# Optimization experiments

Measured on AMD Instinct MI355X. Metric: run time of the kernel, lower is better.

The kernel has to match this reference:

```python
import jax, jax.numpy as jnp
import numpy as np

HIDDEN = 16
ROUNDS = 5


def _mlp2(x, W1, b1, W2, b2):
    # features-first MLP: x [in, E] -> [out, E]
    h = jax.nn.relu(W1 @ x + b1[:, None])
    return W2 @ h + b2[:, None]


def setup_inputs() -> dict:
    key = jax.random.key(0)
    ks = jax.random.split(key, 20)
    n_nodes, n_edges, n_bi, h = 100_000, 1_000_000, 500_000, HIDDEN

    def lin(k, o, i):
        return (jax.random.normal(k, (o, i), jnp.float32) / float(np.sqrt(i)))

    inp = {
        "nodes": jax.random.normal(ks[0], (n_nodes,), jnp.float32),
        "edges": jax.random.normal(ks[1], (n_edges,), jnp.float32),
        "receivers": jax.random.randint(ks[2], (n_edges,), 0, n_nodes),
        "senders": jax.random.randint(ks[3], (n_edges,), 0, n_nodes),
        "bi_edges_indx": jax.random.randint(ks[4], (2, n_bi), 0, n_edges),
        # NodeEncoder: 1 -> h -> h
        "node_enc_W1": lin(ks[5], h, 1), "node_enc_b1": jnp.zeros(h, jnp.float32),
        "node_enc_W2": lin(ks[6], h, h), "node_enc_b2": jnp.zeros(h, jnp.float32),
        # EdgeEncoder: 1 -> h -> h
        "edge_enc_W1": lin(ks[7], h, 1), "edge_enc_b1": jnp.zeros(h, jnp.float32),
        "edge_enc_W2": lin(ks[8], h, h), "edge_enc_b2": jnp.zeros(h, jnp.float32),
        # MessagePass (per-round weights): edge update 3h->h->h, node update 2h->h->h
        "mp_edge_W1": jax.random.normal(ks[9], (ROUNDS, h, 3 * h), jnp.float32) / float(np.sqrt(3 * h)),
        "mp_edge_b1": jnp.zeros((ROUNDS, h), jnp.float32),
        "mp_edge_W2": jax.random.normal(ks[10], (ROUNDS, h, h), jnp.float32) / float(np.sqrt(h)),
        "mp_edge_b2": jnp.zeros((ROUNDS, h), jnp.float32),
        "mp_node_W1": jax.random.normal(ks[11], (ROUNDS, h, 2 * h), jnp.float32) / float(np.sqrt(2 * h)),
        "mp_node_b1": jnp.zeros((ROUNDS, h), jnp.float32),
        "mp_node_W2": jax.random.normal(ks[12], (ROUNDS, h, h), jnp.float32) / float(np.sqrt(h)),
        "mp_node_b2": jnp.zeros((ROUNDS, h), jnp.float32),
        # EdgeDecoder: h -> h -> 1
        "edge_dec_W1": lin(ks[13], h, h), "edge_dec_b1": jnp.zeros(h, jnp.float32),
        "edge_dec_W2": lin(ks[14], 1, h), "edge_dec_b2": jnp.zeros(1, jnp.float32),
    }
    return inp


def reference(nodes, edges, receivers, senders, bi_edges_indx,
              node_enc_W1, node_enc_b1, node_enc_W2, node_enc_b2,
              edge_enc_W1, edge_enc_b1, edge_enc_W2, edge_enc_b2,
              mp_edge_W1, mp_edge_b1, mp_edge_W2, mp_edge_b2,
              mp_node_W1, mp_node_b1, mp_node_W2, mp_node_b2,
              edge_dec_W1, edge_dec_b1, edge_dec_W2, edge_dec_b2):
    n_nodes = nodes.shape[0]
    # encode (features-first layout, eqx Linear semantics W @ x)
    nf = _mlp2(nodes[None, :], node_enc_W1, node_enc_b1, node_enc_W2, node_enc_b2)  # [h, n_nodes]
    ef = _mlp2(edges[None, :], edge_enc_W1, edge_enc_b1, edge_enc_W2, edge_enc_b2)  # [h, n_edges]

    ones = jnp.ones((ef.shape[1],), ef.dtype)
    deg = jnp.maximum(jax.ops.segment_sum(ones, receivers, num_segments=n_nodes), 1.0)

    for r in range(ROUNDS):
        # edge update: gather sender/receiver node feats, MLP on concat [3h, E]
        msg_in = jnp.concatenate([nf[:, senders], nf[:, receivers], ef], axis=0)
        ef = _mlp2(msg_in, mp_edge_W1[r], mp_edge_b1[r], mp_edge_W2[r], mp_edge_b2[r])
        # node update: scatter-average incoming edges then MLP on concat [2h, N]
        agg = jax.ops.segment_sum(ef.T, receivers, num_segments=n_nodes).T / deg[None, :]
        nf = _mlp2(jnp.concatenate([nf, agg], axis=0), mp_node_W1[r], mp_node_b1[r], mp_node_W2[r], mp_node_b2[r])

    # bidirectional edge averaging: avg (i->j, j->i) pairs
    i, j = bi_edges_indx[0], bi_edges_indx[1]
    avg = 0.5 * (ef[:, i] + ef[:, j])
    ef = ef.at[:, i].set(avg).at[:, j].set(avg)

    # decode to scalar edge values, squeeze
    vals = _mlp2(ef, edge_dec_W1, edge_dec_b1, edge_dec_W2, edge_dec_b2)[0]  # [n_edges]

    # graph_tril: keep lower-triangular entries (row=receiver >= col=sender), zero the rest
    vals = jnp.where(receivers >= senders, vals, jnp.zeros((), vals.dtype))
    # COO representation of the lower-triangular sparse matrix (data, rows, cols)
    return vals, receivers, senders
```

## Files before the change

### kernel.cpp

```cpp
#include <hip/hip_runtime.h>
#include <hip/hip_bf16.h>

#define H 16
#define NW 20
#define SCAN_TILE 2048

typedef __attribute__((ext_vector_type(8))) short short8;
typedef __attribute__((ext_vector_type(4))) float f32x4;

__device__ __forceinline__ float bf2f(unsigned short u) {
    union { unsigned int u; float f; } c; c.u = ((unsigned int)u) << 16; return c.f;
}

__device__ __forceinline__ unsigned short f2bf(float f) {
    union { float f; unsigned int u; } c; c.f = f;
    unsigned int u = c.u;
    unsigned int r = (u + 0x7fffu + ((u >> 16) & 1u)) >> 16;
    return (unsigned short)r;
}

__device__ __forceinline__ unsigned int packbf2(float a, float b) {
    return (unsigned int)f2bf(a) | ((unsigned int)f2bf(b) << 16);
}

__device__ __forceinline__ void unpack8(uint4 u, float* f) {
    union { unsigned int u; float f; } c;
    c.u = u.x << 16; f[0] = c.f; c.u = u.x & 0xffff0000u; f[1] = c.f;
    c.u = u.y << 16; f[2] = c.f; c.u = u.y & 0xffff0000u; f[3] = c.f;
    c.u = u.z << 16; f[4] = c.f; c.u = u.z & 0xffff0000u; f[5] = c.f;
    c.u = u.w << 16; f[6] = c.f; c.u = u.w & 0xffff0000u; f[7] = c.f;
}

struct WPtrs { const unsigned short* src[NW]; int len[NW]; int off[NW]; };

__global__ void cvt_weights_kernel(WPtrs p, float* __restrict__ dst) {
    int a = blockIdx.x;
    const unsigned short* s = p.src[a];
    float* d = dst + p.off[a];
    int n = p.len[a];
    for (int t = threadIdx.x; t < n; t += blockDim.x) d[t] = bf2f(s[t]);
}

__global__ void mk_frags_kernel(const unsigned short* __restrict__ W1raw,
                                const unsigned short* __restrict__ W2raw,
                                unsigned short* __restrict__ w1a,
                                unsigned short* __restrict__ w2a)
{
    for (int idx = threadIdx.x; idx < 5 * 2 * 64 * 8; idx += blockDim.x) {
        int j = idx & 7, l = (idx >> 3) & 63, c = (idx >> 9) & 1, r = idx >> 10;
        int m = l & 15, quad = l >> 4;
        int k = c * 32 + quad * 8 + j;
        w1a[idx] = (k < 48) ? W1raw[(r * 16 + m) * 48 + k] : (unsigned short)0;
    }
    for (int idx = threadIdx.x; idx < 5 * 64 * 8; idx += blockDim.x) {
        int j = idx & 7, l = (idx >> 3) & 63, r = idx >> 9;
        int m = l & 15, quad = l >> 4;
        int k = quad * 8 + j;
        w2a[idx] = (k < 16) ? W2raw[(r * 16 + m) * 16 + k] : (unsigned short)0;
    }
}

__global__ __launch_bounds__(256) void encode_node_kernel(
    const unsigned short* __restrict__ xin, int n,
    const float* __restrict__ W1, const float* __restrict__ b1,
    const float* __restrict__ W2, const float* __restrict__ b2,
    unsigned short* __restrict__ out)
{
    int i = blockIdx.x * blockDim.x + threadIdx.x;
    if (i >= n) return;
    float v = bf2f(xin[i]);
    float h[H];
    #pragma unroll
    for (int o = 0; o < H; ++o) {
        float t = W1[o] * v + b1[o];
        h[o] = t > 0.f ? t : 0.f;
    }
    float acc[H];
    #pragma unroll
    for (int o = 0; o < H; ++o) acc[o] = b2[o];
    #pragma unroll
    for (int k = 0; k < H; ++k) {
        float hk = h[k];
        #pragma unroll
        for (int o = 0; o < H; ++o) acc[o] += W2[o * H + k] * hk;
    }
    uint4 o0, o1;
    o0.x = packbf2(acc[0], acc[1]);  o0.y = packbf2(acc[2], acc[3]);
    o0.z = packbf2(acc[4], acc[5]);  o0.w = packbf2(acc[6], acc[7]);
    o1.x = packbf2(acc[8], acc[9]);  o1.y = packbf2(acc[10], acc[11]);
    o1.z = packbf2(acc[12], acc[13]); o1.w = packbf2(acc[14], acc[15]);
    uint4* dst = (uint4*)(out + (size_t)i * H);
    dst[0] = o0; dst[1] = o1;
}

__global__ __launch_bounds__(256) void encode_edge_kernel(
    const unsigned short* __restrict__ edges, const int* __restrict__ elist, int n_edges,
    const float* __restrict__ W1, const float* __restrict__ b1,
    const float* __restrict__ W2, const float* __restrict__ b2,
    unsigned short* __restrict__ efb)
{
    int pos = blockIdx.x * blockDim.x + threadIdx.x;
    if (pos >= n_edges) return;
    float v = bf2f(edges[elist[pos]]);
    float h[H];
    #pragma unroll
    for (int o = 0; o < H; ++o) {
        float t = W1[o] * v + b1[o];
        h[o] = t > 0.f ? t : 0.f;
    }
    float acc[H];
    #pragma unroll
    for (int o = 0; o < H; ++o) acc[o] = b2[o];
    #pragma unroll
    for (int k = 0; k < H; ++k) {
        float hk = h[k];
        #pragma unroll
        for (int o = 0; o < H; ++o) acc[o] += W2[o * H + k] * hk;
    }
    uint4 o0, o1;
    o0.x = packbf2(acc[0], acc[1]);  o0.y = packbf2(acc[2], acc[3]);
    o0.z = packbf2(acc[4], acc[5]);  o0.w = packbf2(acc[6], acc[7]);
    o1.x = packbf2(acc[8], acc[9]);  o1.y = packbf2(acc[10], acc[11]);
    o1.z = packbf2(acc[12], acc[13]); o1.w = packbf2(acc[14], acc[15]);
    uint4* dst = (uint4*)(efb + (size_t)pos * H);
    dst[0] = o0; dst[1] = o1;
}

__global__ __launch_bounds__(256) void hist_kernel(
    const int* __restrict__ recv, int n_edges, int* __restrict__ cnt)
{
    int e = blockIdx.x * blockDim.x + threadIdx.x;
    if (e < n_edges) atomicAdd(&cnt[recv[e]], 1);
}

__global__ __launch_bounds__(256) void scan_part_kernel(
    const int* __restrict__ cnt, int n, int* __restrict__ blocksum)
{
    int base = blockIdx.x * SCAN_TILE + threadIdx.x * 8;
    int s = 0;
    #pragma unroll
    for (int k = 0; k < 8; ++k) { int i = base + k; if (i < n) s += cnt[i]; }
    __shared__ int red[256];
    red[threadIdx.x] = s;
    __syncthreads();
    for (int off = 128; off > 0; off >>= 1) {
        if (threadIdx.x < off) red[threadIdx.x] += red[threadIdx.x + off];
        __syncthreads();
    }
    if (threadIdx.x == 0) blocksum[blockIdx.x] = red[0];
}

__global__ __launch_bounds__(1024) void scan_blocksums_kernel(
    int* __restrict__ blocksum, int nb, int n, int* __restrict__ row_start)
{
    __shared__ int sums[1024];
    int t = threadIdx.x;
    int v = (t < nb) ? blocksum[t] : 0;
    sums[t] = v;
    __syncthreads();
    for (int off = 1; off < 1024; off <<= 1) {
        int u = (t >= off) ? sums[t - off] : 0;
        __syncthreads();
        sums[t] += u;
        __syncthreads();
    }
    if (t < nb) blocksum[t] = sums[t] - v;
    if (t == 1023) row_start[n] = sums[1023];
}

__global__ __launch_bounds__(256) void scan_final_kernel(
    const int* __restrict__ cnt, int n, const int* __restrict__ blocksum,
    int* __restrict__ row_start, int* __restrict__ cursor)
{
    int t = threadIdx.x;
    int base = blockIdx.x * SCAN_TILE + t * 8;
    int loc[8]; int s = 0;
    #pragma unroll
    for (int k = 0; k < 8; ++k) { int i = base + k; loc[k] = (i < n) ? cnt[i] : 0; s += loc[k]; }
    __shared__ int sums[256];
    sums[t] = s;
    __syncthreads();
    for (int off = 1; off < 256; off <<= 1) {
        int u = (t >= off) ? sums[t - off] : 0;
        __syncthreads();
        sums[t] += u;
        __syncthreads();
    }
    int run = blocksum[blockIdx.x] + sums[t] - s;
    #pragma unroll
    for (int k = 0; k < 8; ++k) {
        int i = base + k;
        if (i < n) { row_start[i] = run; cursor[i] = run; run += loc[k]; }
    }
}

__global__ __launch_bounds__(256) void fill_kernel(
    const int* __restrict__ recv, const int* __restrict__ send, int n_edges,
    int* __restrict__ cursor, int* __restrict__ elist, int* __restrict__ ipos,
    int* __restrict__ s_perm, int* __restrict__ r_perm)
{
    int e = blockIdx.x * blockDim.x + threadIdx.x;
    if (e >= n_edges) return;
    int r = recv[e];
    int pos = atomicAdd(&cursor[r], 1);
    elist[pos] = e;
    ipos[e] = pos;
    s_perm[pos] = send[e];
    r_perm[pos] = r;
}

__global__ __launch_bounds__(256) void edge_update_mfma(
    const unsigned short* __restrict__ nfb, unsigned short* __restrict__ efb,
    const int* __restrict__ s_perm, const int* __restrict__ r_perm, int n_edges,
    const unsigned short* __restrict__ w1a, const unsigned short* __restrict__ w2a,
    const float* __restrict__ b1, const float* __restrict__ b2)
{
    __shared__ uint4 Xs[8 * 256];
    __shared__ uint4 Hs[4 * 4 * 16];

    const int t = threadIdx.x;
    const int lane = t & 63;
    const int wave = t >> 6;
    const int quad = lane >> 4;
    const int nn = lane & 15;
    const int base = blockIdx.x * 256;

    const short8 wa0 = *(const short8*)(w1a + (size_t)lane * 8);
    const short8 wa1 = *(const short8*)(w1a + 512 + (size_t)lane * 8);
    const short8 wa2 = *(const short8*)(w2a + (size_t)lane * 8);
    const float4 bv1 = *(const float4*)(b1 + quad * 4);
    const float4 bv2 = *(const float4*)(b2 + quad * 4);

    int pos = base + t;
    int cp = pos < n_edges ? pos : n_edges - 1;
    int s = s_perm[cp], r = r_perm[cp];
    const uint4* pns = (const uint4*)(nfb + (size_t)s * H);
    const uint4* pnr = (const uint4*)(nfb + (size_t)r * H);
    const uint4* pef = (const uint4*)(efb + (size_t)cp * H);
    uint4 a0 = pns[0], a1 = pns[1];
    uint4 r0 = pnr[0], r1 = pnr[1];
    uint4 c0 = pef[0], c1 = pef[1];
    uint4 z; z.x = 0; z.y = 0; z.z = 0; z.w = 0;
    Xs[0 * 256 + t] = a0; Xs[1 * 256 + t] = a1;
    Xs[2 * 256 + t] = r0; Xs[3 * 256 + t] = r1;
    Xs[4 * 256 + t] = c0; Xs[5 * 256 + t] = c1;
    Xs[6 * 256 + t] = z;  Xs[7 * 256 + t] = z;
    if (lane < 32) Hs[wave * 64 + 32 + lane] = z;
    __syncthreads();

    #pragma unroll
    for (int it = 0; it < 4; ++it) {
        int nb = it * 64 + wave * 16 + nn;
        const short8 xb0 = *(const short8*)&Xs[quad * 256 + nb];
        const short8 xb1 = *(const short8*)&Xs[(4 + quad) * 256 + nb];
        f32x4 d1 = {0.f, 0.f, 0.f, 0.f};
        d1 = __builtin_amdgcn_mfma_f32_16x16x32_bf16(wa0, xb0, d1, 0, 0, 0);
        d1 = __builtin_amdgcn_mfma_f32_16x16x32_bf16(wa1, xb1, d1, 0, 0, 0);
        float h0 = d1[0] + bv1.x; h0 = h0 > 0.f ? h0 : 0.f;
        float h1 = d1[1] + bv1.y; h1 = h1 > 0.f ? h1 : 0.f;
        float h2 = d1[2] + bv1.z; h2 = h2 > 0.f ? h2 : 0.f;
        float h3 = d1[3] + bv1.w; h3 = h3 > 0.f ? h3 : 0.f;
        uint2 hu;
        hu.x = packbf2(h0, h1);
        hu.y = packbf2(h2, h3);
        ((uint2*)Hs)[(wave * 64 + (quad >> 1) * 16 + nn) * 2 + (quad & 1)] = hu;
        __syncthreads();
        const short8 hb = *(const short8*)&Hs[wave * 64 + quad * 16 + nn];
        f32x4 d2 = {0.f, 0.f, 0.f, 0.f};
        d2 = __builtin_amdgcn_mfma_f32_16x16x32_bf16(wa2, hb, d2, 0, 0, 0);
        int edge = base + nb;
        if (edge < n_edges) {
            uint2 ov;
            ov.x = packbf2(d2[0] + bv2.x, d2[1] + bv2.y);
            ov.y = packbf2(d2[2] + bv2.z, d2[3] + bv2.w);
            ((uint2*)efb)[(size_t)edge * 4 + quad] = ov;
        }
        __syncthreads();
    }
}

__global__ __launch_bounds__(256) void node_update_kernel(
    unsigned short* __restrict__ nfb, const unsigned short* __restrict__ ef,
    const int* __restrict__ row_start, int n_nodes,
    const float* __restrict__ W1, const float* __restrict__ b1,
    const float* __restrict__ W2, const float* __restrict__ b2)
{
    int i = blockIdx.x * blockDim.x + threadIdx.x;
    if (i >= n_nodes) return;
    int lo = row_start[i], hi = row_start[i + 1];
    float a[H];
    #pragma unroll
    for (int o = 0; o < H; ++o) a[o] = 0.f;
    for (int j = lo; j < hi; ++j) {
        const uint4* pe = (const uint4*)(ef + (size_t)j * H);
        uint4 u0 = pe[0], u1 = pe[1];
        float f[H];
        unpack8(u0, f);
        unpack8(u1, f + 8);
        #pragma unroll
        for (int o = 0; o < H; ++o) a[o] += f[o];
    }
    int d = hi - lo;
    float rd = 1.0f / (float)(d > 1 ? d : 1);

    const uint4* pn = (const uint4*)(nfb + (size_t)i * H);
    uint4 n0 = pn[0], n1 = pn[1];
    float xn[H];
    unpack8(n0, xn);
    unpack8(n1, xn + 8);

    float h[H];
    #pragma unroll
    for (int o = 0; o < H; ++o) h[o] = b1[o];
    #pragma unroll
    for (int k = 0; k < H; ++k) {
        float xk = xn[k];
        #pragma unroll
        for (int o = 0; o < H; ++o) h[o] += W1[o * 32 + k] * xk;
    }
    #pragma unroll
    for (int k = 0; k < H; ++k) {
        float xk = a[k] * rd;
        #pragma unroll
        for (int o = 0; o < H; ++o) h[o] += W1[o * 32 + 16 + k] * xk;
    }
    #pragma unroll
    for (int o = 0; o < H; ++o) h[o] = h[o] > 0.f ? h[o] : 0.f;
    float acc[H];
    #pragma unroll
    for (int o = 0; o < H; ++o) acc[o] = b2[o];
    #pragma unroll
    for (int k = 0; k < H; ++k) {
        float hk = h[k];
        #pragma unroll
        for (int o = 0; o < H; ++o) acc[o] += W2[o * H + k] * hk;
    }
    uint4 o0, o1;
    o0.x = packbf2(acc[0], acc[1]);  o0.y = packbf2(acc[2], acc[3]);
    o0.z = packbf2(acc[4], acc[5]);  o0.w = packbf2(acc[6], acc[7]);
    o1.x = packbf2(acc[8], acc[9]);  o1.y = packbf2(acc[10], acc[11]);
    o1.z = packbf2(acc[12], acc[13]); o1.w = packbf2(acc[14], acc[15]);
    uint4* dst = (uint4*)(nfb + (size_t)i * H);
    dst[0] = o0; dst[1] = o1;
}

__global__ __launch_bounds__(256) void bi_avg_kernel(
    unsigned short* __restrict__ ef, const int* __restrict__ ipos,
    const int* __restrict__ bi, int n_bi)
{
    int p = blockIdx.x * blockDim.x + threadIdx.x;
    if (p >= n_bi) return;
    int i = ipos[bi[p]], j = ipos[bi[n_bi + p]];
    uint4* pi = (uint4*)(ef + (size_t)i * H);
    uint4* pj = (uint4*)(ef + (size_t)j * H);
    uint4 a0 = pi[0], a1 = pi[1], b0 = pj[0], b1 = pj[1];
    float fa[H], fb[H];
    unpack8(a0, fa); unpack8(a1, fa + 8);
    unpack8(b0, fb); unpack8(b1, fb + 8);
    float m[H];
    #pragma unroll
    for (int o = 0; o < H; ++o) m[o] = 0.5f * (fa[o] + fb[o]);
    uint4 o0, o1;
    o0.x = packbf2(m[0], m[1]);  o0.y = packbf2(m[2], m[3]);
    o0.z = packbf2(m[4], m[5]);  o0.w = packbf2(m[6], m[7]);
    o1.x = packbf2(m[8], m[9]);  o1.y = packbf2(m[10], m[11]);
    o1.z = packbf2(m[12], m[13]); o1.w = packbf2(m[14], m[15]);
    pi[0] = o0; pi[1] = o1;
    pj[0] = o0; pj[1] = o1;
}

__global__ __launch_bounds__(256) void decode_kernel(
    const unsigned short* __restrict__ ef, const int* __restrict__ ipos,
    const int* __restrict__ recv, const int* __restrict__ send, int n_edges,
    const float* __restrict__ W1, const float* __restrict__ b1,
    const float* __restrict__ W2, const float* __restrict__ b2,
    float* __restrict__ out)
{
    int e = blockIdx.x * blockDim.x + threadIdx.x;
    if (e >= n_edges) return;
    int pos = ipos[e];
    const uint4* pe = (const uint4*)(ef + (size_t)pos * H);
    uint4 u0 = pe[0], u1 = pe[1];
    float x[H];
    unpack8(u0, x);
    unpack8(u1, x + 8);
    float h[H];
    #pragma unroll
    for (int o = 0; o < H; ++o) h[o] = b1[o];
    #pragma unroll
    for (int k = 0; k < H; ++k) {
        float xk = x[k];
        #pragma unroll
        for (int o = 0; o < H; ++o) h[o] += W1[o * H + k] * xk;
    }
    float val = b2[0];
    #pragma unroll
    for (int k = 0; k < H; ++k) {
        float hk = h[k] > 0.f ? h[k] : 0.f;
        val += W2[k] * hk;
    }
    int r = recv[e], s = send[e];
    val = (r >= s) ? val : 0.0f;
    out[e] = val;
    out[(size_t)n_edges + e] = bf2f(f2bf((float)r));
    out[2 * (size_t)n_edges + e] = bf2f(f2bf((float)s));
}

extern "C" void kernel_launch(void* const* d_in, const int* in_sizes, int n_in,
                              void* d_out, int out_size, void* d_ws, size_t ws_size,
                              hipStream_t stream) {
    const unsigned short* nodes = (const unsigned short*)d_in[0];
    const unsigned short* edges = (const unsigned short*)d_in[1];
    const int* receivers = (const int*)d_in[2];
    const int* senders   = (const int*)d_in[3];
    const int* bi        = (const int*)d_in[4];
    const int n_nodes = in_sizes[0];
    const int n_edges = in_sizes[1];
    const int n_bi    = in_sizes[4] / 2;

    static const int wl[NW] = {16,16,256,16, 16,16,256,16,
                               3840,80,1280,80, 2560,80,1280,80,
                               256,16,16,1};
    WPtrs wp;
    {
        int off = 0;
        for (int a = 0; a < NW; ++a) {
            wp.src[a] = (const unsigned short*)d_in[5 + a];
            wp.len[a] = wl[a];
            wp.off[a] = off;
            off += wl[a];
        }
    }
    float* wf = (float*)d_ws;
    const float* Wf[NW];
    for (int a = 0; a < NW; ++a) Wf[a] = wf + wp.off[a];

    unsigned short* w1a = (unsigned short*)(wf + 10240);
    unsigned short* w2a = w1a + 5 * 2 * 64 * 8;
    unsigned short* nfb = w2a + 5 * 64 * 8;
    unsigned short* efb = nfb + (size_t)n_nodes * H;
    int* cnt       = (int*)(efb + (size_t)n_edges * H);
    int* row_start = cnt + n_nodes;
    int* cursor    = row_start + n_nodes + 1;
    int* elist     = cursor + n_nodes;
    int* ipos      = elist + n_edges;
    int* s_perm    = ipos + n_edges;
    int* r_perm    = s_perm + n_edges;
    int* blocksum  = r_perm + n_edges;

    const int bn = 256;
    const int nb_scan = (n_nodes + SCAN_TILE - 1) / SCAN_TILE;
    const int nb_edge = (n_edges + bn - 1) / bn;

    cvt_weights_kernel<<<NW, 256, 0, stream>>>(wp, wf);
    mk_frags_kernel<<<1, 256, 0, stream>>>(
        (const unsigned short*)d_in[13], (const unsigned short*)d_in[15], w1a, w2a);
    encode_node_kernel<<<(n_nodes + bn - 1) / bn, bn, 0, stream>>>(
        nodes, n_nodes, Wf[0], Wf[1], Wf[2], Wf[3], nfb);

    hipMemsetAsync(cnt, 0, (size_t)n_nodes * 4, stream);
    hist_kernel<<<nb_edge, bn, 0, stream>>>(receivers, n_edges, cnt);
    scan_part_kernel<<<nb_scan, 256, 0, stream>>>(cnt, n_nodes, blocksum);
    scan_blocksums_kernel<<<1, 1024, 0, stream>>>(blocksum, nb_scan, n_nodes, row_start);
    scan_final_kernel<<<nb_scan, 256, 0, stream>>>(cnt, n_nodes, blocksum, row_start, cursor);
    fill_kernel<<<nb_edge, bn, 0, stream>>>(
        receivers, senders, n_edges, cursor, elist, ipos, s_perm, r_perm);

    encode_edge_kernel<<<nb_edge, bn, 0, stream>>>(
        edges, elist, n_edges, Wf[4], Wf[5], Wf[6], Wf[7], efb);

    for (int r = 0; r < 5; ++r) {
        edge_update_mfma<<<nb_edge, bn, 0, stream>>>(
            nfb, efb, s_perm, r_perm, n_edges,
            w1a + r * 1024, w2a + r * 512,
            Wf[9] + r * H, Wf[11] + r * H);
        node_update_kernel<<<(n_nodes + bn - 1) / bn, bn, 0, stream>>>(
            nfb, efb, row_start, n_nodes,
            Wf[12] + r * 2 * H * H, Wf[13] + r * H,
            Wf[14] + r * H * H,     Wf[15] + r * H);
    }

    bi_avg_kernel<<<(n_bi + bn - 1) / bn, bn, 0, stream>>>(efb, ipos, bi, n_bi);
    decode_kernel<<<nb_edge, bn, 0, stream>>>(
        efb, ipos, receivers, senders, n_edges,
        Wf[16], Wf[17], Wf[18], Wf[19], (float*)d_out);
}
```

Before: 514.7 us.

## Fuse segment aggregation into edge update kernel via shared-memory partial sums

The edge-update kernel now writes its bf16 outputs into shared memory and sums edges per receiver within each 256-edge block, writing fp32 partials to an agg buffer. Receivers whose edge range lies entirely inside the block get a plain store; ranges that cross a block boundary use atomics. The node update then reads the 16 precomputed sums per node instead of walking its CSR edge list over efb. The sender is now fetched indirectly through elist and senders instead of a materialised s_perm, and r_perm is built by a separate expand kernel. In exchange, each round adds a memset of agg and an extra indirection in the edge kernel, and boundary atomics make the summation order vary between runs.

```diff
diff --git a/kernel.cpp b/kernel.cpp
--- a/kernel.cpp
+++ b/kernel.cpp
@@ -93,6 +93,94 @@
     dst[0] = o0; dst[1] = o1;
 }
 
+__global__ __launch_bounds__(256) void hist_kernel(
+    const int* __restrict__ recv, int n_edges, int* __restrict__ cnt)
+{
+    int e = blockIdx.x * blockDim.x + threadIdx.x;
+    if (e < n_edges) atomicAdd(&cnt[recv[e]], 1);
+}
+
+__global__ __launch_bounds__(256) void scan_part_kernel(
+    const int* __restrict__ cnt, int n, int* __restrict__ blocksum)
+{
+    int base = blockIdx.x * SCAN_TILE + threadIdx.x * 8;
+    int s = 0;
+    #pragma unroll
+    for (int k = 0; k < 8; ++k) { int i = base + k; if (i < n) s += cnt[i]; }
+    __shared__ int red[256];
+    red[threadIdx.x] = s;
+    __syncthreads();
+    for (int off = 128; off > 0; off >>= 1) {
+        if (threadIdx.x < off) red[threadIdx.x] += red[threadIdx.x + off];
+        __syncthreads();
+    }
+    if (threadIdx.x == 0) blocksum[blockIdx.x] = red[0];
+}
+
+__global__ __launch_bounds__(1024) void scan_blocksums_kernel(
+    int* __restrict__ blocksum, int nb, int n, int* __restrict__ row_start)
+{
+    __shared__ int sums[1024];
+    int t = threadIdx.x;
+    int v = (t < nb) ? blocksum[t] : 0;
+    sums[t] = v;
+    __syncthreads();
+    for (int off = 1; off < 1024; off <<= 1) {
+        int u = (t >= off) ? sums[t - off] : 0;
+        __syncthreads();
+        sums[t] += u;
+        __syncthreads();
+    }
+    if (t < nb) blocksum[t] = sums[t] - v;
+    if (t == 1023) row_start[n] = sums[1023];
+}
+
+__global__ __launch_bounds__(256) void scan_final_kernel(
+    const int* __restrict__ cnt, int n, const int* __restrict__ blocksum,
+    int* __restrict__ row_start, int* __restrict__ cursor)
+{
+    int t = threadIdx.x;
+    int base = blockIdx.x * SCAN_TILE + t * 8;
+    int loc[8]; int s = 0;
+    #pragma unroll
+    for (int k = 0; k < 8; ++k) { int i = base + k; loc[k] = (i < n) ? cnt[i] : 0; s += loc[k]; }
+    __shared__ int sums[256];
+    sums[t] = s;
+    __syncthreads();
+    for (int off = 1; off < 256; off <<= 1) {
+        int u = (t >= off) ? sums[t - off] : 0;
+        __syncthreads();
+        sums[t] += u;
+        __syncthreads();
+    }
+    int run = blocksum[blockIdx.x] + sums[t] - s;
+    #pragma unroll
+    for (int k = 0; k < 8; ++k) {
+        int i = base + k;
+        if (i < n) { row_start[i] = run; cursor[i] = run; run += loc[k]; }
+    }
+}
+
+__global__ __launch_bounds__(256) void expand_r_kernel(
+    const int* __restrict__ row_start, int n_nodes, int* __restrict__ r_perm)
+{
+    int i = blockIdx.x * blockDim.x + threadIdx.x;
+    if (i >= n_nodes) return;
+    int lo = row_start[i], hi = row_start[i + 1];
+    for (int p = lo; p < hi; ++p) r_perm[p] = i;
+}
+
+__global__ __launch_bounds__(256) void fill_kernel(
+    const int* __restrict__ recv, int n_edges,
+    int* __restrict__ cursor, int* __restrict__ ipos, int* __restrict__ elist)
+{
+    int e = blockIdx.x * blockDim.x + threadIdx.x;
+    if (e >= n_edges) return;
+    int pos = atomicAdd(&cursor[recv[e]], 1);
+    ipos[e] = pos;
+    elist[pos] = e;
+}
+
 __global__ __launch_bounds__(256) void encode_edge_kernel(
     const unsigned short* __restrict__ edges, const int* __restrict__ elist, int n_edges,
     const float* __restrict__ W1, const float* __restrict__ b1,
@@ -126,92 +214,11 @@
     dst[0] = o0; dst[1] = o1;
 }
 
-__global__ __launch_bounds__(256) void hist_kernel(
-    const int* __restrict__ recv, int n_edges, int* __restrict__ cnt)
-{
-    int e = blockIdx.x * blockDim.x + threadIdx.x;
-    if (e < n_edges) atomicAdd(&cnt[recv[e]], 1);
-}
-
-__global__ __launch_bounds__(256) void scan_part_kernel(
-    const int* __restrict__ cnt, int n, int* __restrict__ blocksum)
-{
-    int base = blockIdx.x * SCAN_TILE + threadIdx.x * 8;
-    int s = 0;
-    #pragma unroll
-    for (int k = 0; k < 8; ++k) { int i = base + k; if (i < n) s += cnt[i]; }
-    __shared__ int red[256];
-    red[threadIdx.x] = s;
-    __syncthreads();
-    for (int off = 128; off > 0; off >>= 1) {
-        if (threadIdx.x < off) red[threadIdx.x] += red[threadIdx.x + off];
-        __syncthreads();
-    }
-    if (threadIdx.x == 0) blocksum[blockIdx.x] = red[0];
-}
-
-__global__ __launch_bounds__(1024) void scan_blocksums_kernel(
-    int* __restrict__ blocksum, int nb, int n, int* __restrict__ row_start)
-{
-    __shared__ int sums[1024];
-    int t = threadIdx.x;
-    int v = (t < nb) ? blocksum[t] : 0;
-    sums[t] = v;
-    __syncthreads();
-    for (int off = 1; off < 1024; off <<= 1) {
-        int u = (t >= off) ? sums[t - off] : 0;
-        __syncthreads();
-        sums[t] += u;
-        __syncthreads();
-    }
-    if (t < nb) blocksum[t] = sums[t] - v;
-    if (t == 1023) row_start[n] = sums[1023];
-}
-
-__global__ __launch_bounds__(256) void scan_final_kernel(
-    const int* __restrict__ cnt, int n, const int* __restrict__ blocksum,
-    int* __restrict__ row_start, int* __restrict__ cursor)
-{
-    int t = threadIdx.x;
-    int base = blockIdx.x * SCAN_TILE + t * 8;
-    int loc[8]; int s = 0;
-    #pragma unroll
-    for (int k = 0; k < 8; ++k) { int i = base + k; loc[k] = (i < n) ? cnt[i] : 0; s += loc[k]; }
-    __shared__ int sums[256];
-    sums[t] = s;
-    __syncthreads();
-    for (int off = 1; off < 256; off <<= 1) {
-        int u = (t >= off) ? sums[t - off] : 0;
-        __syncthreads();
-        sums[t] += u;
-        __syncthreads();
-    }
-    int run = blocksum[blockIdx.x] + sums[t] - s;
-    #pragma unroll
-    for (int k = 0; k < 8; ++k) {
-        int i = base + k;
-        if (i < n) { row_start[i] = run; cursor[i] = run; run += loc[k]; }
-    }
-}
-
-__global__ __launch_bounds__(256) void fill_kernel(
-    const int* __restrict__ recv, const int* __restrict__ send, int n_edges,
-    int* __restrict__ cursor, int* __restrict__ elist, int* __restrict__ ipos,
-    int* __restrict__ s_perm, int* __restrict__ r_perm)
-{
-    int e = blockIdx.x * blockDim.x + threadIdx.x;
-    if (e >= n_edges) return;
-    int r = recv[e];
-    int pos = atomicAdd(&cursor[r], 1);
-    elist[pos] = e;
-    ipos[e] = pos;
-    s_perm[pos] = send[e];
-    r_perm[pos] = r;
-}
-
 __global__ __launch_bounds__(256) void edge_update_mfma(
     const unsigned short* __restrict__ nfb, unsigned short* __restrict__ efb,
-    const int* __restrict__ s_perm, const int* __restrict__ r_perm, int n_edges,
+    const int* __restrict__ elist, const int* __restrict__ senders,
+    const int* __restrict__ r_perm, const int* __restrict__ row_start,
+    float* __restrict__ agg, int n_edges,
     const unsigned short* __restrict__ w1a, const unsigned short* __restrict__ w2a,
     const float* __restrict__ b1, const float* __restrict__ b2)
 {
@@ -233,7 +240,9 @@
 
     int pos = base + t;
     int cp = pos < n_edges ? pos : n_edges - 1;
-    int s = s_perm[cp], r = r_perm[cp];
+    int e = elist[cp];
+    int s = senders[e];
+    int r = r_perm[cp];
     const uint4* pns = (const uint4*)(nfb + (size_t)s * H);
     const uint4* pnr = (const uint4*)(nfb + (size_t)r * H);
     const uint4* pef = (const uint4*)(efb + (size_t)cp * H);
@@ -268,40 +277,63 @@
         const short8 hb = *(const short8*)&Hs[wave * 64 + quad * 16 + nn];
         f32x4 d2 = {0.f, 0.f, 0.f, 0.f};
         d2 = __builtin_amdgcn_mfma_f32_16x16x32_bf16(wa2, hb, d2, 0, 0, 0);
+        uint2 ov;
+        ov.x = packbf2(d2[0] + bv2.x, d2[1] + bv2.y);
+        ov.y = packbf2(d2[2] + bv2.z, d2[3] + bv2.w);
         int edge = base + nb;
-        if (edge < n_edges) {
-            uint2 ov;
-            ov.x = packbf2(d2[0] + bv2.x, d2[1] + bv2.y);
-            ov.y = packbf2(d2[2] + bv2.z, d2[3] + bv2.w);
+        if (edge < n_edges)
             ((uint2*)efb)[(size_t)edge * 4 + quad] = ov;
+        ((uint2*)Xs)[((quad >> 1) * 256 + nb) * 2 + (quad & 1)] = ov;
+        __syncthreads();
+    }
+
+    int last = (base + 255 < n_edges) ? base + 255 : n_edges - 1;
+    int r_lo = r_perm[base];
+    int r_hi = r_perm[last];
+    int npairs = (r_hi - r_lo + 1) * 2;
+    for (int idx = t; idx < npairs; idx += 256) {
+        int rid = r_lo + (idx >> 1);
+        int half = idx & 1;
+        int lo = row_start[rid], hi = row_start[rid + 1];
+        int lo2 = lo < base ? base : lo;
+        int hi2 = hi > base + 256 ? base + 256 : hi;
+        if (lo2 >= hi2) continue;
+        float acc[8];
+        #pragma unroll
+        for (int k = 0; k < 8; ++k) acc[k] = 0.f;
+        for (int j = lo2 - base; j < hi2 - base; ++j) {
+            uint4 u = Xs[half * 256 + j];
+            float f[8];
+            unpack8(u, f);
+            #pragma unroll
+            for (int k = 0; k < 8; ++k) acc[k] += f[k];
         }
-        __syncthreads();
+        float* dst = agg + (size_t)rid * H + half * 8;
+        if (lo >= base && hi <= base + 256) {
+            ((float4*)dst)[0] = make_float4(acc[0], acc[1], acc[2], acc[3]);
+            ((float4*)dst)[1] = make_float4(acc[4], acc[5], acc[6], acc[7]);
+        } else {
+            #pragma unroll
+            for (int k = 0; k < 8; ++k) atomicAdd(&dst[k], acc[k]);
+        }
     }
 }
 
 __global__ __launch_bounds__(256) void node_update_kernel(
-    unsigned short* __restrict__ nfb, const unsigned short* __restrict__ ef,
+    unsigned short* __restrict__ nfb, const float* __restrict__ agg,
     const int* __restrict__ row_start, int n_nodes,
     const float* __restrict__ W1, const float* __restrict__ b1,
     const float* __restrict__ W2, const float* __restrict__ b2)
 {
     int i = blockIdx.x * blockDim.x + threadIdx.x;
     if (i >= n_nodes) return;
-    int lo = row_start[i], hi = row_start[i + 1];
-    float a[H];
-    #pragma unroll
-    for (int o = 0; o < H; ++o) a[o] = 0.f;
-    for (int j = lo; j < hi; ++j) {
-        const uint4* pe = (const uint4*)(ef + (size_t)j * H);
-        uint4 u0 = pe[0], u1 = pe[1];
-        float f[H];
-        unpack8(u0, f);
-        unpack8(u1, f + 8);
-        #pragma unroll
-        for (int o = 0; o < H; ++o) a[o] += f[o];
-    }
-    int d = hi - lo;
+    int d = row_start[i + 1] - row_start[i];
     float rd = 1.0f / (float)(d > 1 ? d : 1);
+
+    const float4* pa = (const float4*)(agg + (size_t)i * H);
+    float4 a0 = pa[0], a1 = pa[1], a2 = pa[2], a3 = pa[3];
+    float a[H] = {a0.x, a0.y, a0.z, a0.w, a1.x, a1.y, a1.z, a1.w,
+                  a2.x, a2.y, a2.z, a2.w, a3.x, a3.y, a3.z, a3.w};
 
     const uint4* pn = (const uint4*)(nfb + (size_t)i * H);
     uint4 n0 = pn[0], n1 = pn[1];
@@ -439,23 +471,24 @@
     unsigned short* w2a = w1a + 5 * 2 * 64 * 8;
     unsigned short* nfb = w2a + 5 * 64 * 8;
     unsigned short* efb = nfb + (size_t)n_nodes * H;
-    int* cnt       = (int*)(efb + (size_t)n_edges * H);
+    float* agg     = (float*)(efb + (size_t)n_edges * H);
+    int* cnt       = (int*)(agg + (size_t)n_nodes * H);
     int* row_start = cnt + n_nodes;
     int* cursor    = row_start + n_nodes + 1;
-    int* elist     = cursor + n_nodes;
-    int* ipos      = elist + n_edges;
-    int* s_perm    = ipos + n_edges;
-    int* r_perm    = s_perm + n_edges;
+    int* ipos      = cursor + n_nodes;
+    int* elist     = ipos + n_edges;
+    int* r_perm    = elist + n_edges;
     int* blocksum  = r_perm + n_edges;
 
     const int bn = 256;
     const int nb_scan = (n_nodes + SCAN_TILE - 1) / SCAN_TILE;
     const int nb_edge = (n_edges + bn - 1) / bn;
+    const int nb_node = (n_nodes + bn - 1) / bn;
 
     cvt_weights_kernel<<<NW, 256, 0, stream>>>(wp, wf);
     mk_frags_kernel<<<1, 256, 0, stream>>>(
         (const unsigned short*)d_in[13], (const unsigned short*)d_in[15], w1a, w2a);
-    encode_node_kernel<<<(n_nodes + bn - 1) / bn, bn, 0, stream>>>(
+    encode_node_kernel<<<nb_node, bn, 0, stream>>>(
         nodes, n_nodes, Wf[0], Wf[1], Wf[2], Wf[3], nfb);
 
     hipMemsetAsync(cnt, 0, (size_t)n_nodes * 4, stream);
@@ -463,19 +496,19 @@
     scan_part_kernel<<<nb_scan, 256, 0, stream>>>(cnt, n_nodes, blocksum);
     scan_blocksums_kernel<<<1, 1024, 0, stream>>>(blocksum, nb_scan, n_nodes, row_start);
     scan_final_kernel<<<nb_scan, 256, 0, stream>>>(cnt, n_nodes, blocksum, row_start, cursor);
-    fill_kernel<<<nb_edge, bn, 0, stream>>>(
-        receivers, senders, n_edges, cursor, elist, ipos, s_perm, r_perm);
-
+    expand_r_kernel<<<nb_node, bn, 0, stream>>>(row_start, n_nodes, r_perm);
+    fill_kernel<<<nb_edge, bn, 0, stream>>>(receivers, n_edges, cursor, ipos, elist);
     encode_edge_kernel<<<nb_edge, bn, 0, stream>>>(
         edges, elist, n_edges, Wf[4], Wf[5], Wf[6], Wf[7], efb);
 
     for (int r = 0; r < 5; ++r) {
+        hipMemsetAsync(agg, 0, (size_t)n_nodes * H * 4, stream);
         edge_update_mfma<<<nb_edge, bn, 0, stream>>>(
-            nfb, efb, s_perm, r_perm, n_edges,
+            nfb, efb, elist, senders, r_perm, row_start, agg, n_edges,
             w1a + r * 1024, w2a + r * 512,
             Wf[9] + r * H, Wf[11] + r * H);
-        node_update_kernel<<<(n_nodes + bn - 1) / bn, bn, 0, stream>>>(
-            nfb, efb, row_start, n_nodes,
+        node_update_kernel<<<nb_node, bn, 0, stream>>>(
+            nfb, agg, row_start, n_nodes,
             Wf[12] + r * 2 * H * H, Wf[13] + r * H,
             Wf[14] + r * H * H,     Wf[15] + r * H);
     }
```

After: 610.0 us. 18.5% more time.
